# Kernel optimization log

Hardware: AMD Instinct MI355X
Metric: run time of the kernel (lower is better)

## Reference

```python
import jax, jax.numpy as jnp
import numpy as np

TEMPERATURE = 0.07
EPS = 1e-8
LAMBDA_CONTRASTIVE = 0.3
AMBIGUOUS_THRESHOLD = 0.05
LABEL_SMOOTHING = 0.1

B, D, NUM_DIMS, NUM_PIECES = 4096, 256, 19, 1024


def setup_inputs() -> dict:
    key = jax.random.key(0)
    ks = jax.random.split(key, 7)
    return {
        "z_a": jax.random.normal(ks[0], (B, D), dtype=jnp.float32),
        "z_b": jax.random.normal(ks[1], (B, D), dtype=jnp.float32),
        "ranking_logits": jax.random.normal(ks[2], (B, NUM_DIMS), dtype=jnp.float32),
        "labels_a": jax.random.uniform(ks[3], (B, NUM_DIMS), dtype=jnp.float32),
        "labels_b": jax.random.uniform(ks[4], (B, NUM_DIMS), dtype=jnp.float32),
        "piece_ids_a": jax.random.randint(ks[5], (B,), 0, NUM_PIECES, dtype=jnp.int64 if jax.config.jax_enable_x64 else jnp.int32),
        "piece_ids_b": jax.random.randint(ks[6], (B,), 0, NUM_PIECES, dtype=jnp.int64 if jax.config.jax_enable_x64 else jnp.int32),
    }


def _infonce(embeddings, piece_ids, temperature=TEMPERATURE, eps=EPS):
    # embeddings [N, D], piece_ids [N]. Same-piece samples are positives.
    norm = jnp.sqrt(jnp.sum(embeddings * embeddings, axis=-1, keepdims=True))
    z = embeddings / jnp.maximum(norm, eps)  # F.normalize semantics
    sim = (z @ z.T) / temperature  # [N, N]
    n = sim.shape[0]
    eye = jnp.eye(n, dtype=bool)
    piece_mask = piece_ids[None, :] == piece_ids[:, None]
    pos_mask = piece_mask & ~eye
    neg_mask = (~piece_mask) & ~eye
    # row-wise max subtraction (detached in torch) is a no-op on the value since
    # (pos - logsumexp) is shift-invariant; compute stably via masked logsumexp.
    neg_inf = jnp.array(-jnp.inf, sim.dtype)
    neg_lse = jax.scipy.special.logsumexp(jnp.where(neg_mask, sim, neg_inf), axis=-1)  # [N]
    valid_anchor = pos_mask.any(axis=1) & neg_mask.any(axis=1)  # [N]
    pair_mask = pos_mask & valid_anchor[:, None]  # each positive of a valid anchor
    # per-positive term: logsumexp([pos_sim, negs_of_row]) - pos_sim
    lse = jnp.logaddexp(sim, neg_lse[:, None])  # [N, N]
    term = jnp.where(pair_mask, lse - sim, 0.0)
    count = jnp.sum(pair_mask)
    loss = jnp.sum(term) / jnp.maximum(count, 1)
    return jnp.where(count > 0, loss, 0.0)


def _ranking_loss(logits, labels_a, labels_b,
                  ambiguous_threshold=AMBIGUOUS_THRESHOLD,
                  label_smoothing=LABEL_SMOOTHING):
    label_diff = labels_a - labels_b
    targets = (label_diff > 0).astype(logits.dtype)
    non_ambiguous = jnp.abs(label_diff) >= ambiguous_threshold
    targets = targets * (1.0 - label_smoothing) + 0.5 * label_smoothing
    # BCE-with-logits, elementwise, mean over non-ambiguous entries
    bce = jnp.maximum(logits, 0.0) - logits * targets + jnp.log1p(jnp.exp(-jnp.abs(logits)))
    cnt = jnp.sum(non_ambiguous)
    loss = jnp.sum(jnp.where(non_ambiguous, bce, 0.0)) / jnp.maximum(cnt, 1)
    return jnp.where(cnt > 0, loss, 0.0)


def reference(z_a, z_b, ranking_logits, labels_a, labels_b, piece_ids_a, piece_ids_b):
    l_rank = _ranking_loss(ranking_logits, labels_a, labels_b)
    all_z = jnp.concatenate([z_a, z_b], axis=0)        # [2B, D]
    all_pieces = jnp.concatenate([piece_ids_a, piece_ids_b], axis=0)  # [2B]
    l_contrast = _infonce(all_z, all_pieces)
    total = l_rank + LAMBDA_CONTRASTIVE * l_contrast
    return (total, l_rank, l_contrast)
```

## Files before the change

kernel.cpp:

```cpp
#include <hip/hip_runtime.h>
#include <hip/hip_bf16.h>
#include <math.h>

#define NTOT 8192
#define HB   4096
#define DIM  256
#define RANK_N (4096*19)
#define NORM_BLOCKS (NTOT/4)
#define RANK_BLOCKS (RANK_N/256)
#define ZERO_BLOCKS 2
#define INV_T 14.285714285714286f
#define SHIFT 16.0f
#define C1 20.609592f
#define C2 23.083120f
#define MAXP  48
#define POST_BLOCKS (NTOT/256)

typedef __attribute__((ext_vector_type(8))) short bf16x8_t;
typedef __attribute__((ext_vector_type(4))) float f32x4_t;

__device__ __forceinline__ unsigned short f2bf(float f) {
  union { float fv; unsigned int u; } v; v.fv = f;
  unsigned int u = v.u;
  unsigned int r = u + 0x7FFFu + ((u >> 16) & 1u);
  return (unsigned short)(r >> 16);
}

__device__ __forceinline__ const float* zrow(const float* za, const float* zb, int g) {
  return g < HB ? za + (size_t)g * DIM : zb + (size_t)(g - HB) * DIM;
}
__device__ __forceinline__ int piece_of(const int* pa, const int* pb, int g) {
  return g < HB ? pa[g] : pb[g - HB];
}

__device__ __forceinline__ void gload_lds16(const unsigned short* g, unsigned short* l) {
  __builtin_amdgcn_global_load_lds(
      (const __attribute__((address_space(1))) unsigned int*)g,
      (__attribute__((address_space(3))) unsigned int*)l, 16, 0, 0);
}

__global__ void k_pre(const float* __restrict__ za, const float* __restrict__ zb,
                      const float* __restrict__ logits, const float* __restrict__ la,
                      const float* __restrict__ lb,
                      const int* __restrict__ pa, const int* __restrict__ pb,
                      unsigned short* __restrict__ zn, float* __restrict__ rank_part,
                      float* __restrict__ neg_s, int* __restrict__ posCount,
                      float* __restrict__ accf, int* __restrict__ done) {
  __shared__ float sred[8];
  int bid = blockIdx.x;
  int t = threadIdx.x;
  if (bid < NORM_BLOCKS) {
    int lane = t & 63, w = t >> 6;
    int row = bid * 4 + w;
    const float* src = zrow(za, zb, row);
    float4 v = *reinterpret_cast<const float4*>(src + lane * 4);
    float ss = v.x * v.x + v.y * v.y + v.z * v.z + v.w * v.w;
    for (int o = 32; o; o >>= 1) ss += __shfl_xor(ss, o, 64);
    float inv = 1.0f / fmaxf(sqrtf(ss), 1e-8f);
    ushort4 o;
    o.x = f2bf(v.x * inv); o.y = f2bf(v.y * inv);
    o.z = f2bf(v.z * inv); o.w = f2bf(v.w * inv);
    int phys = (((lane >> 1) ^ (row & 7)) << 3) + ((lane & 1) << 2);
    *reinterpret_cast<ushort4*>(zn + (size_t)row * DIM + phys) = o;
  } else if (bid < NORM_BLOCKS + RANK_BLOCKS) {
    int rb = bid - NORM_BLOCKS;
    int e = rb * 256 + t;
    float lsum = 0.f, lcnt = 0.f;
    float diff = la[e] - lb[e];
    if (fabsf(diff) >= 0.05f) {
      float x = logits[e];
      float tgt = diff > 0.f ? 0.95f : 0.05f;
      lsum = fmaxf(x, 0.f) - x * tgt + log1pf(__expf(-fabsf(x)));
      lcnt = 1.f;
    }
    for (int o = 32; o; o >>= 1) { lsum += __shfl_xor(lsum, o, 64); lcnt += __shfl_xor(lcnt, o, 64); }
    int w = t >> 6, lane = t & 63;
    if (lane == 0) { sred[w * 2] = lsum; sred[w * 2 + 1] = lcnt; }
    __syncthreads();
    if (t == 0) {
      float S = 0.f, C = 0.f;
      for (int i = 0; i < 4; ++i) { S += sred[i * 2]; C += sred[i * 2 + 1]; }
      rank_part[rb * 2] = S;
      rank_part[rb * 2 + 1] = C;
    }
  } else {
    int z = bid - NORM_BLOCKS - RANK_BLOCKS;
    if (z == 0) {
      for (int k = t; k < NTOT; k += 256) neg_s[k] = 0.f;
      if (t == 0) { accf[0] = 0.f; accf[1] = 0.f; accf[2] = 0.f; accf[3] = 0.f; *done = 0; }
    } else {
      for (int k = t; k < NTOT; k += 256) posCount[k] = 0;
    }
  }
}

__global__ __launch_bounds__(256, 4)
void k_gram(const unsigned short* __restrict__ zn,
            const int* __restrict__ pa, const int* __restrict__ pb,
            float* __restrict__ neg_s, int* __restrict__ posCount,
            float* __restrict__ pos_sims) {
  __shared__ unsigned short Bs[2][32 * 256];
  const int t = threadIdx.x;
  const int lane = t & 63;
  const int w = t >> 6;
  const int l15 = lane & 15;
  const int lg = lane >> 4;
  const int it = blockIdx.x >> 4;
  const int chunk = blockIdx.x & 15;
  const int ibase = it * 128;
  const int jbase0 = chunk * 512;

  const int jt0raw = 4 * it - 16 * chunk;
  const int jt0 = jt0raw > 0 ? jt0raw : 0;
  if (jt0 >= 16) return;
  const int dthr = jt0raw + 4;

  bf16x8_t afrag[2][8];
#pragma unroll
  for (int mt = 0; mt < 2; ++mt) {
    int garow = ibase + w * 32 + mt * 16 + l15;
    const unsigned short* asrc = zn + (size_t)garow * DIM;
    int sw = garow & 7;
#pragma unroll
    for (int ks = 0; ks < 8; ++ks)
      afrag[mt][ks] = *reinterpret_cast<const bf16x8_t*>(asrc + (((lg + ks * 4) ^ sw) << 3));
  }

  int prow[8];
#pragma unroll
  for (int mt = 0; mt < 2; ++mt)
#pragma unroll
    for (int r = 0; r < 4; ++r)
      prow[mt * 4 + r] = piece_of(pa, pb, ibase + w * 32 + mt * 16 + lg * 4 + r);

  float s[8] = {0.f, 0.f, 0.f, 0.f, 0.f, 0.f, 0.f, 0.f};

  const int srow = w * 8 + (lane >> 5);
  const int scol = (lane & 31) * 8;

#define STAGE(buf, jt_)                                                        \
  {                                                                            \
    int jb_ = jbase0 + (jt_) * 32;                                             \
    const unsigned short* g0 = zn + (size_t)(jb_ + srow) * DIM + scol;         \
    unsigned short* l0 = &Bs[buf][w * 2048];                                   \
    _Pragma("unroll")                                                          \
    for (int i_ = 0; i_ < 4; ++i_)                                             \
      gload_lds16(g0 + (size_t)(2 * i_) * DIM, l0 + i_ * 512);                 \
  }

  STAGE(0, jt0)
  __syncthreads();

  int cur = 0;
  for (int jt = jt0; jt < 16; ++jt) {
    if (jt < 15) STAGE(cur ^ 1, jt + 1)
    const bool docol = (jt >= dthr);
    const unsigned short* Bb = &Bs[cur][0];
#pragma unroll
    for (int ct = 0; ct < 2; ++ct) {
      int jj = jbase0 + jt * 32 + ct * 16 + l15;
      int pc = piece_of(pa, pb, jj);
      int brow = ct * 16 + l15;
      int bsw = brow & 7;
      const unsigned short* bbase = Bb + brow * 256;
      f32x4_t acc0 = {0.f, 0.f, 0.f, 0.f};
      f32x4_t acc1 = {0.f, 0.f, 0.f, 0.f};
#pragma unroll
      for (int ks = 0; ks < 8; ++ks) {
        bf16x8_t bfrag = *reinterpret_cast<const bf16x8_t*>(bbase + (((lg + ks * 4) ^ bsw) << 3));
        acc0 = __builtin_amdgcn_mfma_f32_16x16x32_bf16(afrag[0][ks], bfrag, acc0, 0, 0, 0);
        acc1 = __builtin_amdgcn_mfma_f32_16x16x32_bf16(afrag[1][ks], bfrag, acc1, 0, 0, 0);
      }
      float ecol = 0.f;
#pragma unroll
      for (int r = 0; r < 4; ++r) {
        int gi0 = ibase + w * 32 + lg * 4 + r;
        if (pc != prow[r]) {
          float e = exp2f(acc0[r] * C1 - C2);
          s[r] += e;
          ecol += e;
        } else if (docol) {
          float sim = acc0[r] * INV_T;
          int s0 = atomicAdd(&posCount[gi0], 1);
          if (s0 < MAXP) pos_sims[(size_t)gi0 * MAXP + s0] = sim;
          int s1 = atomicAdd(&posCount[jj], 1);
          if (s1 < MAXP) pos_sims[(size_t)jj * MAXP + s1] = sim;
        } else if (jj != gi0) {
          int s0 = atomicAdd(&posCount[gi0], 1);
          if (s0 < MAXP) pos_sims[(size_t)gi0 * MAXP + s0] = acc0[r] * INV_T;
        }
        int gi1 = gi0 + 16;
        if (pc != prow[4 + r]) {
          float e = exp2f(acc1[r] * C1 - C2);
          s[4 + r] += e;
          ecol += e;
        } else if (docol) {
          float sim = acc1[r] * INV_T;
          int s0 = atomicAdd(&posCount[gi1], 1);
          if (s0 < MAXP) pos_sims[(size_t)gi1 * MAXP + s0] = sim;
          int s1 = atomicAdd(&posCount[jj], 1);
          if (s1 < MAXP) pos_sims[(size_t)jj * MAXP + s1] = sim;
        } else if (jj != gi1) {
          int s0 = atomicAdd(&posCount[gi1], 1);
          if (s0 < MAXP) pos_sims[(size_t)gi1 * MAXP + s0] = acc1[r] * INV_T;
        }
      }
      if (docol) {
        ecol += __shfl_xor(ecol, 16, 64);
        ecol += __shfl_xor(ecol, 32, 64);
        if (lane < 16) atomicAdd(&neg_s[jj], ecol);
      }
    }
    __syncthreads();
    cur ^= 1;
  }
#pragma unroll
  for (int q = 0; q < 8; ++q) {
    float v = s[q];
    v += __shfl_xor(v, 1, 64);
    v += __shfl_xor(v, 2, 64);
    v += __shfl_xor(v, 4, 64);
    v += __shfl_xor(v, 8, 64);
    if (l15 == 0)
      atomicAdd(&neg_s[ibase + w * 32 + (q >> 2) * 16 + lg * 4 + (q & 3)], v);
  }
#undef STAGE
}

__global__ void k_post(const float* __restrict__ neg_s,
                       const int* __restrict__ posCount, const float* __restrict__ pos_sims,
                       const float* __restrict__ rank_part,
                       float* __restrict__ accf, int* __restrict__ done,
                       float* __restrict__ out) {
  int t = threadIdx.x;
  int i = blockIdx.x * 256 + t;
  float lsum = 0.f, lcnt = 0.f;
  int posCnt = posCount[i];
  if (posCnt > 0 && posCnt < NTOT - 1) {
    float nlse = SHIFT + logf(neg_s[i]);
    int m = posCnt < MAXP ? posCnt : MAXP;
    for (int s = 0; s < m; ++s) {
      float x = nlse - pos_sims[(size_t)i * MAXP + s];
      lsum += fmaxf(x, 0.f) + log1pf(__expf(-fabsf(x)));
    }
    lcnt = (float)posCnt;
  }
  for (int o = 32; o; o >>= 1) { lsum += __shfl_xor(lsum, o, 64); lcnt += __shfl_xor(lcnt, o, 64); }
  __shared__ float sred[8];
  __shared__ int isLast;
  int w = t >> 6, lane = t & 63;
  if (lane == 0) { sred[w * 2] = lsum; sred[w * 2 + 1] = lcnt; }
  __syncthreads();
  if (t == 0) {
    float S = 0.f, C = 0.f;
    for (int k = 0; k < 4; ++k) { S += sred[k * 2]; C += sred[k * 2 + 1]; }
    atomicAdd(&accf[2], S);
    atomicAdd(&accf[3], C);
    __threadfence();
    int old = atomicAdd(done, 1);
    isLast = (old == POST_BLOCKS - 1);
  }
  __syncthreads();
  if (isLast) {
    __threadfence();
    float rs = 0.f, rc = 0.f;
    for (int rb = t; rb < RANK_BLOCKS; rb += 256) {
      rs += rank_part[rb * 2];
      rc += rank_part[rb * 2 + 1];
    }
    for (int o = 32; o; o >>= 1) { rs += __shfl_xor(rs, o, 64); rc += __shfl_xor(rc, o, 64); }
    if (lane == 0) { sred[w * 2] = rs; sred[w * 2 + 1] = rc; }
    __syncthreads();
    if (t == 0) {
      float RS = 0.f, RC = 0.f;
      for (int k = 0; k < 4; ++k) { RS += sred[k * 2]; RC += sred[k * 2 + 1]; }
      float ps = accf[2], pcn = accf[3];
      float l_rank = RC > 0.f ? RS / RC : 0.f;
      float l_con = pcn > 0.f ? ps / pcn : 0.f;
      out[0] = l_rank + 0.3f * l_con;
      out[1] = l_rank;
      out[2] = l_con;
    }
  }
}

extern "C" void kernel_launch(void* const* d_in, const int* in_sizes, int n_in,
                              void* d_out, int out_size, void* d_ws, size_t ws_size,
                              hipStream_t stream) {
  const float* za     = (const float*)d_in[0];
  const float* zb     = (const float*)d_in[1];
  const float* logits = (const float*)d_in[2];
  const float* la     = (const float*)d_in[3];
  const float* lb     = (const float*)d_in[4];
  const int*   pa     = (const int*)d_in[5];
  const int*   pb     = (const int*)d_in[6];
  float* out = (float*)d_out;

  float* wsf = (float*)d_ws;
  int*   wsi = (int*)d_ws;
  float* accf      = wsf;
  int*   done      = wsi + 4;
  float* rank_part = wsf + 8;
  float* neg_s     = wsf + 616;
  int*   posCount  = wsi + 8808;
  float* pos_sims  = wsf + 17000;
  unsigned short* zn = (unsigned short*)(wsf + 410216);

  k_pre<<<NORM_BLOCKS + RANK_BLOCKS + ZERO_BLOCKS, 256, 0, stream>>>(
      za, zb, logits, la, lb, pa, pb, zn, rank_part, neg_s, posCount, accf, done);
  k_gram<<<1024, 256, 0, stream>>>(zn, pa, pb, neg_s, posCount, pos_sims);
  k_post<<<POST_BLOCKS, 256, 0, stream>>>(neg_s, posCount, pos_sims, rank_part, accf, done, out);
}
```

Before: 186.0 us.

## Balance triangular Gram workload by pairing row tiles across fixed-size blocks

The old grid launched 1024 blocks over the upper-triangular Gram matrix, and many of them exited early or did uneven amounts of work. The new mapping pairs row tile p with row tile 63-p so each pair covers a constant number of 32-column steps. That combined span is split into 26 blocks of 10 steps each, giving a 832-block grid with equal work per block. A block can cross from one row tile to the other mid-loop, so it reloads the A fragments and flushes the partial row sums with atomics at that boundary. This adds some extra atomics and reloads in exchange for the better load balance and fewer idle blocks.

Measured after the change: 161.4 us. -13.2%, faster.

```diff
diff --git a/kernel.cpp b/kernel.cpp
--- a/kernel.cpp
+++ b/kernel.cpp
@@ -15,6 +15,9 @@
 #define C2 23.083120f
 #define MAXP  48
 #define POST_BLOCKS (NTOT/256)
+#define BPP 26
+#define SPB 10
+#define GRAM_GRID (32*BPP)
 
 typedef __attribute__((ext_vector_type(8))) short bf16x8_t;
 typedef __attribute__((ext_vector_type(4))) float f32x4_t;
@@ -105,60 +108,79 @@
   const int w = t >> 6;
   const int l15 = lane & 15;
   const int lg = lane >> 4;
-  const int it = blockIdx.x >> 4;
-  const int chunk = blockIdx.x & 15;
-  const int ibase = it * 128;
-  const int jbase0 = chunk * 512;
-
-  const int jt0raw = 4 * it - 16 * chunk;
-  const int jt0 = jt0raw > 0 ? jt0raw : 0;
-  if (jt0 >= 16) return;
-  const int dthr = jt0raw + 4;
-
-  bf16x8_t afrag[2][8];
-#pragma unroll
-  for (int mt = 0; mt < 2; ++mt) {
-    int garow = ibase + w * 32 + mt * 16 + l15;
-    const unsigned short* asrc = zn + (size_t)garow * DIM;
-    int sw = garow & 7;
-#pragma unroll
-    for (int ks = 0; ks < 8; ++ks)
-      afrag[mt][ks] = *reinterpret_cast<const bf16x8_t*>(asrc + (((lg + ks * 4) ^ sw) << 3));
-  }
-
-  int prow[8];
-#pragma unroll
-  for (int mt = 0; mt < 2; ++mt)
-#pragma unroll
-    for (int r = 0; r < 4; ++r)
-      prow[mt * 4 + r] = piece_of(pa, pb, ibase + w * 32 + mt * 16 + lg * 4 + r);
-
-  float s[8] = {0.f, 0.f, 0.f, 0.f, 0.f, 0.f, 0.f, 0.f};
+
+  const int p  = blockIdx.x / BPP;
+  const int b  = blockIdx.x % BPP;
+  const int u0 = b * SPB;
+  const int nA = 256 - 4 * p;
+  const int itB = 63 - p;
 
   const int srow = w * 8 + (lane >> 5);
   const int scol = (lane & 31) * 8;
 
-#define STAGE(buf, jt_)                                                        \
+#define J32(u_) ((u_) < nA ? 4 * p + (u_) : 4 * itB + ((u_) - nA))
+
+#define STAGE(buf, j32_)                                                       \
   {                                                                            \
-    int jb_ = jbase0 + (jt_) * 32;                                             \
-    const unsigned short* g0 = zn + (size_t)(jb_ + srow) * DIM + scol;         \
+    const unsigned short* g0 = zn + (size_t)((j32_) * 32 + srow) * DIM + scol; \
     unsigned short* l0 = &Bs[buf][w * 2048];                                   \
     _Pragma("unroll")                                                          \
     for (int i_ = 0; i_ < 4; ++i_)                                             \
       gload_lds16(g0 + (size_t)(2 * i_) * DIM, l0 + i_ * 512);                 \
   }
 
-  STAGE(0, jt0)
+#define FLUSH()                                                                \
+  {                                                                            \
+    _Pragma("unroll")                                                          \
+    for (int q = 0; q < 8; ++q) {                                              \
+      float v = s[q];                                                          \
+      v += __shfl_xor(v, 1, 64);                                               \
+      v += __shfl_xor(v, 2, 64);                                               \
+      v += __shfl_xor(v, 4, 64);                                               \
+      v += __shfl_xor(v, 8, 64);                                               \
+      if (l15 == 0)                                                            \
+        atomicAdd(&neg_s[ibase + w * 32 + (q >> 2) * 16 + lg * 4 + (q & 3)], v); \
+    }                                                                          \
+  }
+
+  bf16x8_t afrag[2][8];
+  int prow[8];
+  float s[8];
+  int curIt = -1, ibase = 0;
+
+  STAGE(0, J32(u0))
   __syncthreads();
 
   int cur = 0;
-  for (int jt = jt0; jt < 16; ++jt) {
-    if (jt < 15) STAGE(cur ^ 1, jt + 1)
-    const bool docol = (jt >= dthr);
+  for (int u = u0; u < u0 + SPB; ++u) {
+    if (u + 1 < u0 + SPB) STAGE(cur ^ 1, J32(u + 1))
+    const int it = (u < nA) ? p : itB;
+    const int j32 = J32(u);
+    if (it != curIt) {
+      if (curIt >= 0) FLUSH()
+      curIt = it;
+      ibase = it * 128;
+#pragma unroll
+      for (int mt = 0; mt < 2; ++mt) {
+        int garow = ibase + w * 32 + mt * 16 + l15;
+        const unsigned short* asrc = zn + (size_t)garow * DIM;
+        int sw = garow & 7;
+#pragma unroll
+        for (int ks = 0; ks < 8; ++ks)
+          afrag[mt][ks] = *reinterpret_cast<const bf16x8_t*>(asrc + (((lg + ks * 4) ^ sw) << 3));
+#pragma unroll
+        for (int r = 0; r < 4; ++r)
+          prow[mt * 4 + r] = piece_of(pa, pb, ibase + w * 32 + mt * 16 + lg * 4 + r);
+      }
+#pragma unroll
+      for (int q = 0; q < 8; ++q) s[q] = 0.f;
+    }
+    const bool docol = (j32 >= 4 * it + 4);
+    const int jb = j32 * 32;
     const unsigned short* Bb = &Bs[cur][0];
 #pragma unroll
     for (int ct = 0; ct < 2; ++ct) {
-      int jj = jbase0 + jt * 32 + ct * 16 + l15;
+      int jj = jb + ct * 16 + l15;
       int pc = piece_of(pa, pb, jj);
       int brow = ct * 16 + l15;
       int bsw = brow & 7;
@@ -214,17 +236,10 @@
     __syncthreads();
     cur ^= 1;
   }
-#pragma unroll
-  for (int q = 0; q < 8; ++q) {
-    float v = s[q];
-    v += __shfl_xor(v, 1, 64);
-    v += __shfl_xor(v, 2, 64);
-    v += __shfl_xor(v, 4, 64);
-    v += __shfl_xor(v, 8, 64);
-    if (l15 == 0)
-      atomicAdd(&neg_s[ibase + w * 32 + (q >> 2) * 16 + lg * 4 + (q & 3)], v);
-  }
+  FLUSH()
 #undef STAGE
+#undef FLUSH
+#undef J32
 }
 
 __global__ void k_post(const float* __restrict__ neg_s,
@@ -308,6 +323,6 @@
 
   k_pre<<<NORM_BLOCKS + RANK_BLOCKS + ZERO_BLOCKS, 256, 0, stream>>>(
       za, zb, logits, la, lb, pa, pb, zn, rank_part, neg_s, posCount, accf, done);
-  k_gram<<<1024, 256, 0, stream>>>(zn, pa, pb, neg_s, posCount, pos_sims);
+  k_gram<<<GRAM_GRID, 256, 0, stream>>>(zn, pa, pb, neg_s, posCount, pos_sims);
   k_post<<<POST_BLOCKS, 256, 0, stream>>>(neg_s, posCount, pos_sims, rank_part, accf, done, out);
 }
```
